# Optimization experiments

Hardware: AMD Instinct MI355X
Metric: run time of the kernel (lower is better)

The kernel has to match this reference:

```python
import jax, jax.numpy as jnp
import numpy as np

N_NODES = 50000
N_EDGES = 800000
IN_FEATS = 128
HIDDEN = 128
OUT_FEATS = 2
NUM_GRAPHS = 100


def xavier(key, shape):
    fan_in, fan_out = shape[1], shape[0]
    a = jnp.sqrt(6.0 / (fan_in + fan_out))
    return jax.random.uniform(key, shape, jnp.float32, -a, a)


def setup_inputs() -> dict:
    key = jax.random.key(0)
    ks = jax.random.split(key, 10)
    x = jax.random.normal(ks[0], (N_NODES, IN_FEATS), jnp.float32)
    edge_index = jax.random.randint(ks[1], (2, N_EDGES), 0, N_NODES, jnp.int64)
    edge_weight = jax.random.uniform(ks[2], (N_EDGES,), jnp.float32)
    batch = jnp.sort(jax.random.randint(ks[3], (N_NODES,), 0, NUM_GRAPHS, jnp.int64))
    return {
        "x": x,
        "edge_index": edge_index,
        "edge_weight": edge_weight,
        "batch": batch,
        "W1": xavier(ks[4], (HIDDEN, IN_FEATS)),
        "b1": jnp.zeros((HIDDEN,), jnp.float32),
        "W2": xavier(ks[5], (HIDDEN, HIDDEN)),
        "b2": jnp.zeros((HIDDEN,), jnp.float32),
        "lin1_w": xavier(ks[6], (IN_FEATS, HIDDEN)),
        "lin1_b": jnp.zeros((IN_FEATS,), jnp.float32),
        "lin2_w": xavier(ks[7], (OUT_FEATS, IN_FEATS)),
        "lin2_b": jnp.zeros((OUT_FEATS,), jnp.float32),
    }


def gcn_conv(x, row, col, ew, W, b, n_nodes):
    # PyG GCNConv: symmetric normalization with self-loops already included
    # deg[i] = sum of edge weights into node i
    deg = jax.ops.segment_sum(ew, col, num_segments=n_nodes)
    dinv = jnp.where(deg > 0, jax.lax.rsqrt(deg), 0.0)
    norm = dinv[row] * ew * dinv[col]                      # [E]
    h = x @ W.T                                            # [N, out]
    msg = norm[:, None] * h[row]                           # [E, out]
    out = jax.ops.segment_sum(msg, col, num_segments=n_nodes)
    return out + b


def reference(x, edge_index, edge_weight, batch, W1, b1, W2, b2,
              lin1_w, lin1_b, lin2_w, lin2_b):
    n = x.shape[0]
    # add self-loops with weight 1 (PyG default fill_value=1.0)
    loops = jnp.arange(n, dtype=edge_index.dtype)
    row = jnp.concatenate([edge_index[0], loops])
    col = jnp.concatenate([edge_index[1], loops])
    ew = jnp.concatenate([edge_weight, jnp.ones((n,), edge_weight.dtype)])

    h = jax.nn.relu(gcn_conv(x, row, col, ew, W1, b1, n))
    h = jax.nn.relu(gcn_conv(h, row, col, ew, W2, b2, n))

    # global_mean_pool over graph ids
    sums = jax.ops.segment_sum(h, batch, num_segments=NUM_GRAPHS)
    cnt = jax.ops.segment_sum(jnp.ones((n,), h.dtype), batch, num_segments=NUM_GRAPHS)
    g = sums / jnp.maximum(cnt, 1.0)[:, None]              # [G, hidden]

    # dropout is identity in eval mode
    g = jax.nn.relu(g @ lin1_w.T + lin1_b)
    return g @ lin2_w.T + lin2_b
```

## Files before the change

kernel.cpp:

```cpp
#include <hip/hip_runtime.h>


typedef unsigned long long ull;
typedef short bf16x8 __attribute__((ext_vector_type(8)));
typedef float f32x4 __attribute__((ext_vector_type(4)));

#define BCAP 5120
#define TILE_E 2048

__device__ inline ushort f2bf(float f) {
    unsigned u = __float_as_uint(f);
    unsigned r = (u + 0x7FFF + ((u >> 16) & 1)) >> 16;
    return (ushort)r;
}
__device__ inline void bsplit(float f, ushort& h, ushort& l) {
    h = f2bf(f);
    float hf = __uint_as_float(((unsigned)h) << 16);
    l = f2bf(f - hf);
}
__device__ inline float bflo(unsigned g) { return __uint_as_float(g << 16); }
__device__ inline float bfhi(unsigned g) { return __uint_as_float(g & 0xffff0000u); }

__global__ void k_wsplit(const float* __restrict__ W1, const float* __restrict__ W2,
                         ushort* __restrict__ w1hi, ushort* __restrict__ w1lo,
                         ushort* __restrict__ w2hi, ushort* __restrict__ w2lo,
                         unsigned* __restrict__ cursor) {
    int i = blockIdx.x * blockDim.x + threadIdx.x;
    if (i < 256) cursor[i] = 0;
    if (i < 4096) {
        float4 v = ((const float4*)W1)[i];
        ushort4 h, l;
        bsplit(v.x, h.x, l.x); bsplit(v.y, h.y, l.y);
        bsplit(v.z, h.z, l.z); bsplit(v.w, h.w, l.w);
        ((ushort4*)w1hi)[i] = h; ((ushort4*)w1lo)[i] = l;
    } else if (i < 8192) {
        int j = i - 4096;
        float4 v = ((const float4*)W2)[j];
        ushort4 h, l;
        bsplit(v.x, h.x, l.x); bsplit(v.y, h.y, l.y);
        bsplit(v.z, h.z, l.z); bsplit(v.w, h.w, l.w);
        ((ushort4*)w2hi)[j] = h; ((ushort4*)w2lo)[j] = l;
    }
}

template <int AFP32>
__device__ __forceinline__ void gemm_body(int blk, int t,
                                          const void* __restrict__ Xsrc,
                                          const ushort* __restrict__ whi,
                                          const ushort* __restrict__ wlo,
                                          ushort* __restrict__ Y, int N) {
    int lane = t & 63;
    int wave = t >> 6;
    int quad = lane >> 4;
    int l16  = lane & 15;
    int rowbase = blk * 128 + wave * 32;

    const f32x4 zero = {0.f, 0.f, 0.f, 0.f};
    f32x4 acc[2][8];
#pragma unroll
    for (int i = 0; i < 2; ++i)
#pragma unroll
        for (int j = 0; j < 8; ++j) acc[i][j] = zero;

#pragma unroll
    for (int kc = 0; kc < 128; kc += 32) {
        bf16x8 ah[2];
#pragma unroll
        for (int rt = 0; rt < 2; ++rt) {
            int r0 = rowbase + rt * 16 + l16;
            r0 = r0 < N ? r0 : N - 1;
            if (AFP32) {
                const float* ap = (const float*)Xsrc + (size_t)r0 * 128 + kc + quad * 8;
                float4 a0 = *(const float4*)ap;
                float4 a1 = *(const float4*)(ap + 4);
                bf16x8 v;
                v[0] = (short)f2bf(a0.x); v[1] = (short)f2bf(a0.y);
                v[2] = (short)f2bf(a0.z); v[3] = (short)f2bf(a0.w);
                v[4] = (short)f2bf(a1.x); v[5] = (short)f2bf(a1.y);
                v[6] = (short)f2bf(a1.z); v[7] = (short)f2bf(a1.w);
                ah[rt] = v;
            } else {
                ah[rt] = *(const bf16x8*)((const ushort*)Xsrc + (size_t)r0 * 128 + kc + quad * 8);
            }
        }
#pragma unroll
        for (int ct = 0; ct < 8; ++ct) {
            int boff = (ct * 16 + l16) * 128 + kc + quad * 8;
            bf16x8 bh = *(const bf16x8*)(whi + boff);
            bf16x8 bl = *(const bf16x8*)(wlo + boff);
#pragma unroll
            for (int rt = 0; rt < 2; ++rt) {
                acc[rt][ct] = __builtin_amdgcn_mfma_f32_16x16x32_bf16(ah[rt], bh, acc[rt][ct], 0, 0, 0);
                acc[rt][ct] = __builtin_amdgcn_mfma_f32_16x16x32_bf16(ah[rt], bl, acc[rt][ct], 0, 0, 0);
            }
        }
    }
#pragma unroll
    for (int rt = 0; rt < 2; ++rt) {
#pragma unroll
        for (int r = 0; r < 4; ++r) {
            int rowi = rowbase + rt * 16 + quad * 4 + r;
            if (rowi < N) {
                ushort* yp = Y + (size_t)rowi * 128 + l16;
#pragma unroll
                for (int ct = 0; ct < 8; ++ct)
                    yp[ct * 16] = f2bf(acc[rt][ct][r]);
            }
        }
    }
}

__global__ __launch_bounds__(256, 4) void k_front(const float* __restrict__ x,
                                                  const ushort* __restrict__ w1hi,
                                                  const ushort* __restrict__ w1lo,
                                                  ushort* __restrict__ h1, int N, int gb,
                                                  const int* __restrict__ row,
                                                  const int* __restrict__ col,
                                                  const float* __restrict__ ew,
                                                  ull* __restrict__ edata,
                                                  unsigned* __restrict__ cursor, int E) {
    __shared__ unsigned hist[256];
    __shared__ unsigned gbase[256];
    int b = blockIdx.x;
    if (b < gb) {
        gemm_body<1>(b, threadIdx.x, x, w1hi, w1lo, h1, N);
        return;
    }
    int t = threadIdx.x;
    int e0 = (b - gb) * TILE_E;
    hist[t] = 0;
    __syncthreads();
    int cl[TILE_E / 256];
#pragma unroll
    for (int i = 0; i < TILE_E / 256; ++i) {
        int e = e0 + i * 256 + t;
        int c = e < E ? col[e] : -1;
        cl[i] = c;
        if (c >= 0) atomicAdd(&hist[c >> 8], 1u);
    }
    __syncthreads();
    unsigned h = hist[t];
    if (h) gbase[t] = atomicAdd(&cursor[t], h);
    __syncthreads();
#pragma unroll
    for (int i = 0; i < TILE_E / 256; ++i) {
        int c = cl[i];
        if (c < 0) continue;
        int e = e0 + i * 256 + t;
        unsigned q = (unsigned)rintf(ew[e] * 32768.0f);
        if (q > 32767u) q = 32767u;
        unsigned val = (q << 17) | (unsigned)row[e];
        int bk = c >> 8;
        unsigned off = atomicSub(&hist[bk], 1u) - 1u;
        unsigned dst = gbase[bk] + off;
        if (dst < (unsigned)BCAP)
            edata[(size_t)bk * BCAP + dst] = ((ull)(unsigned)c << 32) | (ull)val;
    }
}

__global__ __launch_bounds__(256) void k_slots(const ull* __restrict__ edata,
                                               const unsigned* __restrict__ cursor,
                                               ull* __restrict__ packed,
                                               unsigned* __restrict__ slots, int N) {
    __shared__ unsigned cnt[256];
    __shared__ unsigned ews[256];
    int b = blockIdx.x, t = threadIdx.x;
    cnt[t] = 0; ews[t] = 0;
    __syncthreads();
    unsigned m = cursor[b];
    if (m > (unsigned)BCAP) m = BCAP;
    const ull* ed = edata + (size_t)b * BCAP;
    for (unsigned k = t; k < m; k += 256) {
        ull pv = ed[k];
        unsigned c = (unsigned)(pv >> 32);
        unsigned val = (unsigned)pv;
        unsigned clc = c & 255u;
        unsigned pos = atomicAdd(&cnt[clc], 1u);
        if (pos < 64u) slots[((size_t)c << 6) + pos] = val;
        atomicAdd(&ews[clc], val >> 17);
    }
    __syncthreads();
    int node = b * 256 + t;
    if (node < N) packed[node] = ((ull)cnt[t] << 32) | (ull)ews[t];
}

__global__ __launch_bounds__(256, 4) void k_gemm2(const ushort* __restrict__ X,
                                                  const ushort* __restrict__ whi,
                                                  const ushort* __restrict__ wlo,
                                                  ushort* __restrict__ Y, int N) {
    gemm_body<0>(blockIdx.x, threadIdx.x, X, whi, wlo, Y, N);
}

__global__ __launch_bounds__(256) void k_agg(const ushort* __restrict__ H,
                                             ushort* __restrict__ Ob,
                                             const ull* __restrict__ packed,
                                             const unsigned* __restrict__ slots,
                                             const float* __restrict__ bias, int N) {
    int wid = __builtin_amdgcn_readfirstlane((blockIdx.x * blockDim.x + threadIdx.x) >> 6);
    int lane = threadIdx.x & 63;
    if (wid >= N) return;
    const unsigned* HU = (const unsigned*)H;
    const unsigned* PU = (const unsigned*)packed;
    const float kq = 3.0517578125e-5f;
    ull pk = packed[wid];
    int cnt = (int)(pk >> 32); cnt = cnt < 64 ? cnt : 64;
    float dsum = (float)(unsigned)(pk & 0xffffffffull) * kq;
    float dc = rsqrtf(1.0f + dsum);
    float dcs = dc * kq;
    const unsigned* SL = slots + ((size_t)wid << 6);
    unsigned gss = HU[(size_t)wid * 64 + lane];
    float ax = dc * dc * bflo(gss), ay = dc * dc * bfhi(gss);
    int c1 = cnt - 1;
    for (int j = 0; j < cnt; j += 8) {
        int j1 = j+1 < c1 ? j+1 : c1, j2 = j+2 < c1 ? j+2 : c1, j3 = j+3 < c1 ? j+3 : c1;
        int j4 = j+4 < c1 ? j+4 : c1, j5 = j+5 < c1 ? j+5 : c1, j6 = j+6 < c1 ? j+6 : c1;
        int j7 = j+7 < c1 ? j+7 : c1;
        unsigned p0 = SL[j],  p1 = SL[j1], p2 = SL[j2], p3 = SL[j3];
        unsigned p4 = SL[j4], p5 = SL[j5], p6 = SL[j6], p7 = SL[j7];
        unsigned s0 = p0 & 0x1FFFFu, s1 = p1 & 0x1FFFFu, s2 = p2 & 0x1FFFFu, s3 = p3 & 0x1FFFFu;
        unsigned s4 = p4 & 0x1FFFFu, s5 = p5 & 0x1FFFFu, s6 = p6 & 0x1FFFFu, s7 = p7 & 0x1FFFFu;
        float q0 = (float)(p0 >> 17);
        float q1 = j+1 < cnt ? (float)(p1 >> 17) : 0.f;
        float q2 = j+2 < cnt ? (float)(p2 >> 17) : 0.f;
        float q3 = j+3 < cnt ? (float)(p3 >> 17) : 0.f;
        float q4 = j+4 < cnt ? (float)(p4 >> 17) : 0.f;
        float q5 = j+5 < cnt ? (float)(p5 >> 17) : 0.f;
        float q6 = j+6 < cnt ? (float)(p6 >> 17) : 0.f;
        float q7 = j+7 < cnt ? (float)(p7 >> 17) : 0.f;
        float d0 = rsqrtf(1.f + (float)PU[2*s0] * kq);
        float d1 = rsqrtf(1.f + (float)PU[2*s1] * kq);
        float d2 = rsqrtf(1.f + (float)PU[2*s2] * kq);
        float d3 = rsqrtf(1.f + (float)PU[2*s3] * kq);
        float d4 = rsqrtf(1.f + (float)PU[2*s4] * kq);
        float d5 = rsqrtf(1.f + (float)PU[2*s5] * kq);
        float d6 = rsqrtf(1.f + (float)PU[2*s6] * kq);
        float d7 = rsqrtf(1.f + (float)PU[2*s7] * kq);
        float w0 = d0 * q0 * dcs, w1 = d1 * q1 * dcs, w2 = d2 * q2 * dcs, w3 = d3 * q3 * dcs;
        float w4 = d4 * q4 * dcs, w5 = d5 * q5 * dcs, w6 = d6 * q6 * dcs, w7 = d7 * q7 * dcs;
        unsigned g0 = HU[(size_t)s0 * 64 + lane];
        unsigned g1 = HU[(size_t)s1 * 64 + lane];
        unsigned g2 = HU[(size_t)s2 * 64 + lane];
        unsigned g3 = HU[(size_t)s3 * 64 + lane];
        unsigned g4 = HU[(size_t)s4 * 64 + lane];
        unsigned g5 = HU[(size_t)s5 * 64 + lane];
        unsigned g6 = HU[(size_t)s6 * 64 + lane];
        unsigned g7 = HU[(size_t)s7 * 64 + lane];
        ax += w0 * bflo(g0); ay += w0 * bfhi(g0);
        ax += w1 * bflo(g1); ay += w1 * bfhi(g1);
        ax += w2 * bflo(g2); ay += w2 * bfhi(g2);
        ax += w3 * bflo(g3); ay += w3 * bfhi(g3);
        ax += w4 * bflo(g4); ay += w4 * bfhi(g4);
        ax += w5 * bflo(g5); ay += w5 * bfhi(g5);
        ax += w6 * bflo(g6); ay += w6 * bfhi(g6);
        ax += w7 * bflo(g7); ay += w7 * bfhi(g7);
    }
    float2 bb = ((const float2*)bias)[lane];
    ax = fmaxf(ax + bb.x, 0.f);
    ay = fmaxf(ay + bb.y, 0.f);
    unsigned pkout = (unsigned)f2bf(ax) | ((unsigned)f2bf(ay) << 16);
    ((unsigned*)Ob)[(size_t)wid * 64 + lane] = pkout;
}

__global__ __launch_bounds__(128) void k_pool(const ushort* __restrict__ Hb,
                                              const int* __restrict__ batch,
                                              float* __restrict__ pooled, int N) {
    int t = threadIdx.x;
    int n0 = blockIdx.x * 64;
    if (n0 >= N) return;
    int n1 = min(n0 + 64, N);
    int cur = batch[n0];
    float acc = 0.f;
    for (int n = n0; n < n1; ++n) {
        int g = batch[n];
        if (g != cur) {
            atomicAdd(&pooled[cur * 128 + t], acc);
            acc = 0.f; cur = g;
        }
        acc += __uint_as_float(((unsigned)Hb[(size_t)n * 128 + t]) << 16);
    }
    atomicAdd(&pooled[cur * 128 + t], acc);
}

__global__ __launch_bounds__(128) void k_mlp(const float* __restrict__ pooled,
                                             const int* __restrict__ batch,
                                             const float* __restrict__ w1,
                                             const float* __restrict__ b1,
                                             const float* __restrict__ w2,
                                             const float* __restrict__ b2,
                                             float* __restrict__ out, int N, int G) {
    __shared__ float pl[128];
    __shared__ float h1[128];
    int g = blockIdx.x, t = threadIdx.x;
    int lo = 0, hi = N;
    while (lo < hi) { int m = (lo + hi) >> 1; if (batch[m] < g) lo = m + 1; else hi = m; }
    int s = lo;
    lo = s; hi = N;
    while (lo < hi) { int m = (lo + hi) >> 1; if (batch[m] < g + 1) lo = m + 1; else hi = m; }
    float cnt = (float)(lo - s);
    pl[t] = pooled[g * 128 + t] / fmaxf(cnt, 1.0f);
    __syncthreads();
    float sum = b1[t];
#pragma unroll 4
    for (int k = 0; k < 128; ++k) sum += w1[t * 128 + k] * pl[k];
    h1[t] = fmaxf(sum, 0.f);
    __syncthreads();
    if (t < 2) {
        float s2 = b2[t];
        for (int k = 0; k < 128; ++k) s2 += w2[t * 128 + k] * h1[k];
        out[g * 2 + t] = s2;
    }
}

extern "C" void kernel_launch(void* const* d_in, const int* in_sizes, int n_in,
                              void* d_out, int out_size, void* d_ws, size_t ws_size,
                              hipStream_t stream) {
    const float* x   = (const float*)d_in[0];
    const int*   ei  = (const int*)d_in[1];
    const float* ew  = (const float*)d_in[2];
    const int* batch = (const int*)d_in[3];
    const float* W1  = (const float*)d_in[4];
    const float* b1  = (const float*)d_in[5];
    const float* W2  = (const float*)d_in[6];
    const float* b2  = (const float*)d_in[7];
    const float* l1w = (const float*)d_in[8];
    const float* l1b = (const float*)d_in[9];
    const float* l2w = (const float*)d_in[10];
    const float* l2b = (const float*)d_in[11];
    float* out = (float*)d_out;

    const int E = in_sizes[2];
    const int N = in_sizes[3];
    const int G = out_size / 2;
    const int Npad = (N + 127) & ~127;
    const int nbk = (N + 255) >> 8;
    const int* row = ei;
    const int* col = ei + E;

    char* p = (char*)d_ws;
    auto alloc = [&](size_t bytes) -> void* {
        void* r = (void*)p;
        p += (bytes + 511) & ~(size_t)511;
        return r;
    };
    ull*     packed = (ull*)alloc((size_t)N * 8);
    unsigned* slots = (unsigned*)alloc((size_t)N * 64 * 4);
    ushort* w1hi  = (ushort*)alloc(16384 * 2);
    ushort* w1lo  = (ushort*)alloc(16384 * 2);
    ushort* w2hi  = (ushort*)alloc(16384 * 2);
    ushort* w2lo  = (ushort*)alloc(16384 * 2);
    ushort* h1    = (ushort*)alloc((size_t)Npad * 128 * 2);
    ushort* hagg  = (ushort*)alloc((size_t)Npad * 128 * 2);
    float* pooled = (float*)alloc((size_t)G * 128 * 4);
    ull*   edata  = (ull*)alloc((size_t)nbk * BCAP * 8);
    unsigned* cursor = (unsigned*)alloc(256 * 4);

    hipMemsetAsync(pooled, 0, (size_t)G * 128 * 4, stream);

    int nbS = (E + TILE_E - 1) / TILE_E;
    int gb = Npad / 128;
    int ab = ((size_t)N * 64 + 255) / 256;
    k_wsplit<<<32, 256, 0, stream>>>(W1, W2, w1hi, w1lo, w2hi, w2lo, cursor);
    k_front<<<gb + nbS, 256, 0, stream>>>(x, w1hi, w1lo, h1, N, gb,
                                          row, col, ew, edata, cursor, E);
    k_slots<<<nbk, 256, 0, stream>>>(edata, cursor, packed, slots, N);
    k_agg<<<ab, 256, 0, stream>>>(h1, hagg, packed, slots, b1, N);
    k_gemm2<<<gb, 256, 0, stream>>>(hagg, w2hi, w2lo, h1, N);
    k_agg<<<ab, 256, 0, stream>>>(h1, hagg, packed, slots, b2, N);
    k_pool<<<(N + 63) / 64, 128, 0, stream>>>(hagg, batch, pooled, N);
    k_mlp<<<G, 128, 0, stream>>>(pooled, batch, l1w, l1b, l2w, l2b, out, N, G);
}
```

Measured before the change: 262.0 us.

## Reorder layer-2 as aggregate-then-GEMM and fuse bias/ReLU/mean-pool into GEMM epilogue

Layer 2 now aggregates neighbours first and applies the W2 GEMM afterwards, which is valid because the aggregation is linear. Bias, ReLU and the graph pooling are fused into the GEMM epilogue through a shared-memory tile, so the separate pool kernel and the write-out of the final node features go away. The bucket sort also moves from 256-node to 128-node bins, giving more k_slots blocks and smaller per-block buckets. Risks: BCAP is halved, so a crowded bin could overflow and drop edges, and the aggregation now runs on bf16-rounded pre-GEMM features, which changes rounding.

```diff
diff --git a/kernel.cpp b/kernel.cpp
--- a/kernel.cpp
+++ b/kernel.cpp
@@ -5,8 +5,9 @@
 typedef short bf16x8 __attribute__((ext_vector_type(8)));
 typedef float f32x4 __attribute__((ext_vector_type(4)));
 
-#define BCAP 5120
+#define BCAP 2560
 #define TILE_E 2048
+#define NBINS 512
 
 __device__ inline ushort f2bf(float f) {
     unsigned u = __float_as_uint(f);
@@ -26,7 +27,7 @@
                          ushort* __restrict__ w2hi, ushort* __restrict__ w2lo,
                          unsigned* __restrict__ cursor) {
     int i = blockIdx.x * blockDim.x + threadIdx.x;
-    if (i < 256) cursor[i] = 0;
+    if (i < NBINS) cursor[i] = 0;
     if (i < 4096) {
         float4 v = ((const float4*)W1)[i];
         ushort4 h, l;
@@ -43,12 +44,15 @@
     }
 }
 
-template <int AFP32>
+template <int AFP32, int POOL>
 __device__ __forceinline__ void gemm_body(int blk, int t,
                                           const void* __restrict__ Xsrc,
                                           const ushort* __restrict__ whi,
                                           const ushort* __restrict__ wlo,
-                                          ushort* __restrict__ Y, int N) {
+                                          ushort* __restrict__ Y, int N,
+                                          const int* __restrict__ batch,
+                                          const float* __restrict__ bias,
+                                          float* __restrict__ pooled) {
     int lane = t & 63;
     int wave = t >> 6;
     int quad = lane >> 4;
@@ -95,18 +99,49 @@
             }
         }
     }
-#pragma unroll
-    for (int rt = 0; rt < 2; ++rt) {
-#pragma unroll
-        for (int r = 0; r < 4; ++r) {
-            int rowi = rowbase + rt * 16 + quad * 4 + r;
-            if (rowi < N) {
-                ushort* yp = Y + (size_t)rowi * 128 + l16;
-#pragma unroll
-                for (int ct = 0; ct < 8; ++ct)
-                    yp[ct * 16] = f2bf(acc[rt][ct][r]);
+    if constexpr (!POOL) {
+#pragma unroll
+        for (int rt = 0; rt < 2; ++rt) {
+#pragma unroll
+            for (int r = 0; r < 4; ++r) {
+                int rowi = rowbase + rt * 16 + quad * 4 + r;
+                if (rowi < N) {
+                    ushort* yp = Y + (size_t)rowi * 128 + l16;
+#pragma unroll
+                    for (int ct = 0; ct < 8; ++ct)
+                        yp[ct * 16] = f2bf(acc[rt][ct][r]);
+                }
             }
         }
+    } else {
+        __shared__ ushort hb[128][132];
+        __shared__ int bs[128];
+        int n0 = blk * 128;
+        if (t < 128) bs[t] = (n0 + t < N) ? batch[n0 + t] : -1;
+#pragma unroll
+        for (int ct = 0; ct < 8; ++ct) {
+            float bb = bias[ct * 16 + l16];
+#pragma unroll
+            for (int rt = 0; rt < 2; ++rt)
+#pragma unroll
+                for (int r = 0; r < 4; ++r) {
+                    int rl = wave * 32 + rt * 16 + quad * 4 + r;
+                    hb[rl][ct * 16 + l16] = f2bf(fmaxf(acc[rt][ct][r] + bb, 0.f));
+                }
+        }
+        __syncthreads();
+        int col = t & 127, half = t >> 7;
+        float a = 0.f; int cur = -2;
+        for (int r = 0; r < 64; ++r) {
+            int row = half * 64 + r;
+            int g = bs[row];
+            if (g != cur) {
+                if (cur >= 0) atomicAdd(&pooled[cur * 128 + col], a);
+                a = 0.f; cur = g;
+            }
+            if (g >= 0) a += __uint_as_float(((unsigned)hb[row][col]) << 16);
+        }
+        if (cur >= 0) atomicAdd(&pooled[cur * 128 + col], a);
     }
 }
 
@@ -119,16 +154,16 @@
                                                   const float* __restrict__ ew,
                                                   ull* __restrict__ edata,
                                                   unsigned* __restrict__ cursor, int E) {
-    __shared__ unsigned hist[256];
-    __shared__ unsigned gbase[256];
+    __shared__ unsigned hist[NBINS];
+    __shared__ unsigned gbase[NBINS];
     int b = blockIdx.x;
     if (b < gb) {
-        gemm_body<1>(b, threadIdx.x, x, w1hi, w1lo, h1, N);
+        gemm_body<1, 0>(b, threadIdx.x, x, w1hi, w1lo, h1, N, nullptr, nullptr, nullptr);
         return;
     }
     int t = threadIdx.x;
     int e0 = (b - gb) * TILE_E;
-    hist[t] = 0;
+    hist[t] = 0; hist[t + 256] = 0;
     __syncthreads();
     int cl[TILE_E / 256];
 #pragma unroll
@@ -136,11 +171,15 @@
         int e = e0 + i * 256 + t;
         int c = e < E ? col[e] : -1;
         cl[i] = c;
-        if (c >= 0) atomicAdd(&hist[c >> 8], 1u);
-    }
-    __syncthreads();
-    unsigned h = hist[t];
-    if (h) gbase[t] = atomicAdd(&cursor[t], h);
+        if (c >= 0) atomicAdd(&hist[c >> 7], 1u);
+    }
+    __syncthreads();
+#pragma unroll
+    for (int i = 0; i < 2; ++i) {
+        int bin = t + i * 256;
+        unsigned h = hist[bin];
+        if (h) gbase[bin] = atomicAdd(&cursor[bin], h);
+    }
     __syncthreads();
 #pragma unroll
     for (int i = 0; i < TILE_E / 256; ++i) {
@@ -150,7 +189,7 @@
         unsigned q = (unsigned)rintf(ew[e] * 32768.0f);
         if (q > 32767u) q = 32767u;
         unsigned val = (q << 17) | (unsigned)row[e];
-        int bk = c >> 8;
+        int bk = c >> 7;
         unsigned off = atomicSub(&hist[bk], 1u) - 1u;
         unsigned dst = gbase[bk] + off;
         if (dst < (unsigned)BCAP)
@@ -162,10 +201,10 @@
                                                const unsigned* __restrict__ cursor,
                                                ull* __restrict__ packed,
                                                unsigned* __restrict__ slots, int N) {
-    __shared__ unsigned cnt[256];
-    __shared__ unsigned ews[256];
+    __shared__ unsigned cnt[128];
+    __shared__ unsigned ews[128];
     int b = blockIdx.x, t = threadIdx.x;
-    cnt[t] = 0; ews[t] = 0;
+    if (t < 128) { cnt[t] = 0; ews[t] = 0; }
     __syncthreads();
     unsigned m = cursor[b];
     if (m > (unsigned)BCAP) m = BCAP;
@@ -174,23 +213,28 @@
         ull pv = ed[k];
         unsigned c = (unsigned)(pv >> 32);
         unsigned val = (unsigned)pv;
-        unsigned clc = c & 255u;
+        unsigned clc = c & 127u;
         unsigned pos = atomicAdd(&cnt[clc], 1u);
         if (pos < 64u) slots[((size_t)c << 6) + pos] = val;
         atomicAdd(&ews[clc], val >> 17);
     }
     __syncthreads();
-    int node = b * 256 + t;
-    if (node < N) packed[node] = ((ull)cnt[t] << 32) | (ull)ews[t];
-}
-
-__global__ __launch_bounds__(256, 4) void k_gemm2(const ushort* __restrict__ X,
-                                                  const ushort* __restrict__ whi,
-                                                  const ushort* __restrict__ wlo,
-                                                  ushort* __restrict__ Y, int N) {
-    gemm_body<0>(blockIdx.x, threadIdx.x, X, whi, wlo, Y, N);
-}
-
+    if (t < 128) {
+        int node = b * 128 + t;
+        if (node < N) packed[node] = ((ull)cnt[t] << 32) | (ull)ews[t];
+    }
+}
+
+__global__ __launch_bounds__(256, 4) void k_gemm2pool(const ushort* __restrict__ X,
+                                                      const ushort* __restrict__ whi,
+                                                      const ushort* __restrict__ wlo,
+                                                      const int* __restrict__ batch,
+                                                      const float* __restrict__ bias,
+                                                      float* __restrict__ pooled, int N) {
+    gemm_body<0, 1>(blockIdx.x, threadIdx.x, X, whi, wlo, nullptr, N, batch, bias, pooled);
+}
+
+template <int RELU>
 __global__ __launch_bounds__(256) void k_agg(const ushort* __restrict__ H,
                                              ushort* __restrict__ Ob,
                                              const ull* __restrict__ packed,
@@ -254,31 +298,13 @@
         ax += w6 * bflo(g6); ay += w6 * bfhi(g6);
         ax += w7 * bflo(g7); ay += w7 * bfhi(g7);
     }
-    float2 bb = ((const float2*)bias)[lane];
-    ax = fmaxf(ax + bb.x, 0.f);
-    ay = fmaxf(ay + bb.y, 0.f);
+    if constexpr (RELU) {
+        float2 bb = ((const float2*)bias)[lane];
+        ax = fmaxf(ax + bb.x, 0.f);
+        ay = fmaxf(ay + bb.y, 0.f);
+    }
     unsigned pkout = (unsigned)f2bf(ax) | ((unsigned)f2bf(ay) << 16);
     ((unsigned*)Ob)[(size_t)wid * 64 + lane] = pkout;
-}
-
-__global__ __launch_bounds__(128) void k_pool(const ushort* __restrict__ Hb,
-                                              const int* __restrict__ batch,
-                                              float* __restrict__ pooled, int N) {
-    int t = threadIdx.x;
-    int n0 = blockIdx.x * 64;
-    if (n0 >= N) return;
-    int n1 = min(n0 + 64, N);
-    int cur = batch[n0];
-    float acc = 0.f;
-    for (int n = n0; n < n1; ++n) {
-        int g = batch[n];
-        if (g != cur) {
-            atomicAdd(&pooled[cur * 128 + t], acc);
-            acc = 0.f; cur = g;
-        }
-        acc += __uint_as_float(((unsigned)Hb[(size_t)n * 128 + t]) << 16);
-    }
-    atomicAdd(&pooled[cur * 128 + t], acc);
 }
 
 __global__ __launch_bounds__(128) void k_mlp(const float* __restrict__ pooled,
@@ -332,7 +358,7 @@
     const int N = in_sizes[3];
     const int G = out_size / 2;
     const int Npad = (N + 127) & ~127;
-    const int nbk = (N + 255) >> 8;
+    const int nbk = (N + 127) >> 7;
     const int* row = ei;
     const int* col = ei + E;
 
@@ -352,7 +378,7 @@
     ushort* hagg  = (ushort*)alloc((size_t)Npad * 128 * 2);
     float* pooled = (float*)alloc((size_t)G * 128 * 4);
     ull*   edata  = (ull*)alloc((size_t)nbk * BCAP * 8);
-    unsigned* cursor = (unsigned*)alloc(256 * 4);
+    unsigned* cursor = (unsigned*)alloc(NBINS * 4);
 
     hipMemsetAsync(pooled, 0, (size_t)G * 128 * 4, stream);
 
@@ -363,9 +389,8 @@
     k_front<<<gb + nbS, 256, 0, stream>>>(x, w1hi, w1lo, h1, N, gb,
                                           row, col, ew, edata, cursor, E);
     k_slots<<<nbk, 256, 0, stream>>>(edata, cursor, packed, slots, N);
-    k_agg<<<ab, 256, 0, stream>>>(h1, hagg, packed, slots, b1, N);
-    k_gemm2<<<gb, 256, 0, stream>>>(hagg, w2hi, w2lo, h1, N);
-    k_agg<<<ab, 256, 0, stream>>>(h1, hagg, packed, slots, b2, N);
-    k_pool<<<(N + 63) / 64, 128, 0, stream>>>(hagg, batch, pooled, N);
+    k_agg<1><<<ab, 256, 0, stream>>>(h1, hagg, packed, slots, b1, N);
+    k_agg<0><<<ab, 256, 0, stream>>>(hagg, h1, packed, slots, nullptr, N);
+    k_gemm2pool<<<gb, 256, 0, stream>>>(h1, w2hi, w2lo, batch, b2, pooled, N);
     k_mlp<<<G, 128, 0, stream>>>(pooled, batch, l1w, l1b, l2w, l2b, out, N, G);
 }
```

Result: faster. 237.8 us (-9.2%).
